# Kernel tuning notes

Hardware: AMD Instinct MI355X
Metric: run time of the kernel (lower is better)

Reference implementation:

```python
import jax, jax.numpy as jnp
import numpy as np

E = 16          # number of experts
K = 2           # top-k routing
D = 1024        # model dim
F = 512         # expert ffn dim
T = 4096        # tokens
C = 2048


def setup_inputs() -> dict:
    key = jax.random.key(0)
    k1, k2, k3, k4, k5, k6 = jax.random.split(key, 6)
    return {
        "hidden_states": jax.random.normal(k1, (T, D), jnp.float32),
        "topk_indices": jax.random.randint(k2, (T, K), 0, E, jnp.int64),
        "topk_weights": jax.random.uniform(k3, (T, K), jnp.float32),
        "w_gate": jax.random.normal(k4, (E, D, F), jnp.float32) * 0.02,
        "w_up": jax.random.normal(k5, (E, D, F), jnp.float32) * 0.02,
        "w_down": jax.random.normal(k6, (E, F, D), jnp.float32) * 0.02,
    }


def reference(hidden_states, topk_indices, topk_weights, w_gate, w_up, w_down):
    Tn, d = hidden_states.shape
    k = topk_indices.shape[1]
    TK = Tn * k

    # ---- dispatch_tokens: group (token, expert) pairs by expert id ----
    flat_e = topk_indices.reshape(-1)                 # [TK] expert id per slot
    flat_w = topk_weights.reshape(-1)                 # [TK]
    flat_t = jnp.arange(TK) // k                      # [TK] source token id
    order = jnp.argsort(flat_e)                       # sort slots by expert
    se, st, sw = flat_e[order], flat_t[order], flat_w[order]
    counts = jnp.bincount(flat_e, length=E)           # tokens per expert
    starts = jnp.cumsum(counts) - counts              # exclusive prefix sum
    pos = jnp.arange(TK) - starts[se]                 # position within expert bucket
    valid = pos < C
    slot = jnp.where(valid, se * C + pos, E * C)      # overflow -> scratch row

    # gather tokens into padded per-expert buffers [E, C, D]
    buf = jnp.zeros((E * C + 1, d), hidden_states.dtype).at[slot].set(hidden_states[st])
    xe = buf[: E * C].reshape(E, C, d)

    # ---- per-expert gated-SiLU MLP via grouped GEMMs ----
    h = jax.nn.silu(jnp.einsum('ecd,edf->ecf', xe, w_gate)) * jnp.einsum('ecd,edf->ecf', xe, w_up)
    ye = jnp.einsum('ecf,efd->ecd', h, w_down).reshape(E * C, d)

    # ---- weighted scatter-add combine (index_add_) ----
    contrib = ye[jnp.minimum(slot, E * C - 1)] * (sw * valid.astype(sw.dtype))[:, None]
    out = jnp.zeros((Tn, d), topk_weights.dtype).at[st].add(contrib)
    return out.astype(hidden_states.dtype)
```

## Files before the change

### kernel.cpp

```cpp
#include <hip/hip_runtime.h>
#include <hip/hip_bf16.h>

constexpr int E_ = 16, K_ = 2, D_ = 1024, F_ = 512, T_ = 4096;
constexpr int TK_ = T_ * K_;
constexpr int CAP_ = 2048;
constexpr int BM_ = 128;
constexpr int ROWS_MAX = 10240;

constexpr size_t SZ_W   = (size_t)E_ * F_ * D_ * 2;
constexpr size_t OFF_WGT  = 0;
constexpr size_t OFF_WUT  = OFF_WGT + SZ_W;
constexpr size_t OFF_WDT  = OFF_WUT + SZ_W;
constexpr size_t OFF_XG   = OFF_WDT + SZ_W;
constexpr size_t SZ_XG  = (size_t)ROWS_MAX * D_ * 2;
constexpr size_t OFF_H    = OFF_XG + SZ_XG;
constexpr size_t SZ_H   = (size_t)ROWS_MAX * F_ * 2;
constexpr size_t OFF_META = OFF_H + SZ_H;

typedef __attribute__((ext_vector_type(8))) short short8;
typedef __attribute__((ext_vector_type(4))) float float4v;

__device__ __forceinline__ unsigned short f2bf(float f) {
  union { float f; unsigned int u; } v; v.f = f;
  unsigned int r = (v.u + 0x7fffu + ((v.u >> 16) & 1u)) >> 16;
  return (unsigned short)r;
}

__device__ __forceinline__ void load_lds16(const unsigned short* g, unsigned short* l) {
  __builtin_amdgcn_global_load_lds(
      (const __attribute__((address_space(1))) unsigned int*)g,
      (__attribute__((address_space(3))) unsigned int*)l,
      16, 0, 0);
}

__global__ void hist_k(const int* __restrict__ idx, int* __restrict__ hist) {
  int i = blockIdx.x * blockDim.x + threadIdx.x;
  if (i < TK_) atomicAdd(&hist[idx[i]], 1);
}

__global__ void scan_k(const int* __restrict__ hist, int* __restrict__ cnt_c,
                       int* __restrict__ off_al, int* __restrict__ ctr) {
  if (threadIdx.x == 0) {
    int run = 0;
    for (int e = 0; e < E_; ++e) {
      int c = hist[e] > CAP_ ? CAP_ : hist[e];
      cnt_c[e] = c; off_al[e] = run; ctr[e] = 0;
      run += (c + BM_ - 1) & ~(BM_ - 1);
    }
  }
}

__global__ void assign_k(const int* __restrict__ idx, const float* __restrict__ tw,
                         const int* __restrict__ off_al, int* __restrict__ ctr,
                         int* __restrict__ row_token, float* __restrict__ row_weight) {
  int i = blockIdx.x * blockDim.x + threadIdx.x;
  if (i >= TK_) return;
  int e = idx[i];
  int r = atomicAdd(&ctr[e], 1);
  if (r < CAP_) {
    int row = off_al[e] + r;
    row_token[row] = i >> 1;
    row_weight[row] = tw[i];
  }
}

__global__ void gather_k(const float* __restrict__ hidden, const int* __restrict__ row_token,
                         unsigned short* __restrict__ Xg) {
  int r = blockIdx.x;
  int tok = row_token[r];
  int c = threadIdx.x * 4;
  ushort4 o;
  if (tok >= 0) {
    float4 v = *(const float4*)(hidden + (size_t)tok * D_ + c);
    o.x = f2bf(v.x); o.y = f2bf(v.y); o.z = f2bf(v.z); o.w = f2bf(v.w);
  } else {
    o.x = 0; o.y = 0; o.z = 0; o.w = 0;
  }
  *(ushort4*)(Xg + (size_t)r * D_ + c) = o;
}

__global__ void transpose_all_k(const float* __restrict__ wg, const float* __restrict__ wu,
                                const float* __restrict__ wd,
                                unsigned short* __restrict__ WgT, unsigned short* __restrict__ WuT,
                                unsigned short* __restrict__ WdT) {
  __shared__ float tile[32][33];
  int z = blockIdx.y;
  int kind = z >> 4, e = z & 15;
  int R = (kind == 2) ? F_ : D_;
  int C = (kind == 2) ? D_ : F_;
  const float* s = ((kind == 0) ? wg : (kind == 1) ? wu : wd) + (size_t)e * R * C;
  unsigned short* d = ((kind == 0) ? WgT : (kind == 1) ? WuT : WdT) + (size_t)e * R * C;
  int tilesX = C >> 5;
  int t = blockIdx.x;
  int r0 = (t / tilesX) * 32, c0 = (t % tilesX) * 32;
  int tr = threadIdx.x >> 3;
  int tc = (threadIdx.x & 7) * 4;
  float4 v = *(const float4*)(s + (size_t)(r0 + tr) * C + (c0 + tc));
  tile[tr][tc + 0] = v.x; tile[tr][tc + 1] = v.y;
  tile[tr][tc + 2] = v.z; tile[tr][tc + 3] = v.w;
  __syncthreads();
  ushort4 o;
  o.x = f2bf(tile[tc + 0][tr]);
  o.y = f2bf(tile[tc + 1][tr]);
  o.z = f2bf(tile[tc + 2][tr]);
  o.w = f2bf(tile[tc + 3][tr]);
  *(ushort4*)(d + (size_t)(c0 + tr) * R + (r0 + tc)) = o;
}


__launch_bounds__(256)
__global__ void gemm1_k(const unsigned short* __restrict__ Xg,
                        const unsigned short* __restrict__ WgT,
                        const unsigned short* __restrict__ WuT,
                        unsigned short* __restrict__ Hbuf,
                        const int* __restrict__ cnt_c, const int* __restrict__ off_al) {
  int bid = blockIdx.x;
  int swz = (bid & 7) * 512 + (bid >> 3);
  int e = swz >> 8, mt = (swz >> 3) & 31, nt = swz & 7;
  int cnt = cnt_c[e];
  if (mt * 64 >= cnt) return;
  int rbase = off_al[e] + mt * 64;

  __shared__ unsigned short lA[2][64 * 64];
  __shared__ unsigned short lBg[2][64 * 64];
  __shared__ unsigned short lBu[2][64 * 64];

  int tid = threadIdx.x, wid = tid >> 6, lane = tid & 63;
  int wm = wid >> 1, wn = wid & 1;
  int quad = lane >> 4, l15 = lane & 15;
  int sw = l15 & 7;

  const unsigned short* gA = Xg + (size_t)rbase * D_;
  const unsigned short* gB0 = WgT + ((size_t)e * F_ + nt * 64) * D_;
  const unsigned short* gB1 = WuT + ((size_t)e * F_ + nt * 64) * D_;

  float4v accg[2][2], accu[2][2];
#pragma unroll
  for (int i = 0; i < 2; ++i)
#pragma unroll
    for (int j = 0; j < 2; ++j) {
      accg[i][j] = (float4v){0.f, 0.f, 0.f, 0.f};
      accu[i][j] = (float4v){0.f, 0.f, 0.f, 0.f};
    }

  auto stage = [&](int buf, int k0) {
#pragma unroll
    for (int it = 0; it < 2; ++it) {
      int fw = it * 256 + wid * 64;
      int f = fw + lane;
      int row = f >> 3, c8 = (f & 7) ^ (row & 7);
      size_t go = (size_t)row * D_ + k0 + c8 * 8;
      load_lds16(gA + go, &lA[buf][fw * 8]);
      load_lds16(gB0 + go, &lBg[buf][fw * 8]);
      load_lds16(gB1 + go, &lBu[buf][fw * 8]);
    }
  };

  stage(0, 0);
  __syncthreads();

  for (int kt = 0; kt < 16; ++kt) {
    int cur = kt & 1;
    if (kt + 1 < 16) stage(cur ^ 1, (kt + 1) * 64);
#pragma unroll
    for (int kc = 0; kc < 2; ++kc) {
      short8 af[2], bg[2], bu[2];
#pragma unroll
      for (int i = 0; i < 2; ++i) {
        int r = wm * 32 + i * 16 + l15;
        af[i] = *(const short8*)&lA[cur][r * 64 + ((kc * 4 + quad) ^ sw) * 8];
      }
#pragma unroll
      for (int j = 0; j < 2; ++j) {
        int n = wn * 32 + j * 16 + l15;
        bg[j] = *(const short8*)&lBg[cur][n * 64 + ((kc * 4 + quad) ^ sw) * 8];
        bu[j] = *(const short8*)&lBu[cur][n * 64 + ((kc * 4 + quad) ^ sw) * 8];
      }
#pragma unroll
      for (int i = 0; i < 2; ++i)
#pragma unroll
        for (int j = 0; j < 2; ++j) {
          accg[i][j] = __builtin_amdgcn_mfma_f32_16x16x32_bf16(af[i], bg[j], accg[i][j], 0, 0, 0);
          accu[i][j] = __builtin_amdgcn_mfma_f32_16x16x32_bf16(af[i], bu[j], accu[i][j], 0, 0, 0);
        }
    }
    __syncthreads();
  }

  int rem = cnt - mt * 64;
#pragma unroll
  for (int i = 0; i < 2; ++i)
#pragma unroll
    for (int j = 0; j < 2; ++j)
#pragma unroll
      for (int r = 0; r < 4; ++r) {
        int row = wm * 32 + i * 16 + quad * 4 + r;
        if (row < rem) {
          float g = accg[i][j][r], u = accu[i][j][r];
          float h = (g / (1.f + __expf(-g))) * u;
          int n = nt * 64 + wn * 32 + j * 16 + l15;
          Hbuf[(size_t)(rbase + row) * F_ + n] = f2bf(h);
        }
      }
}

__launch_bounds__(256)
__global__ void gemm2_k(const unsigned short* __restrict__ Hbuf,
                        const unsigned short* __restrict__ WdT,
                        float* __restrict__ out,
                        const int* __restrict__ cnt_c, const int* __restrict__ off_al,
                        const int* __restrict__ row_token, const float* __restrict__ row_weight) {
  int bid = blockIdx.x;
  int swz = (bid & 7) * 512 + (bid >> 3);
  int e = swz >> 8, mt = (swz >> 3) & 31, nt = swz & 7;
  int cnt = cnt_c[e];
  if (mt * 64 >= cnt) return;
  int rbase = off_al[e] + mt * 64;

  __shared__ unsigned short lA[2][64 * 64];
  __shared__ unsigned short lB[2][128 * 64];

  int tid = threadIdx.x, wid = tid >> 6, lane = tid & 63;
  int wm = wid >> 1, wn = wid & 1;
  int quad = lane >> 4, l15 = lane & 15;
  int sw = l15 & 7;

  const unsigned short* gA = Hbuf + (size_t)rbase * F_;
  const unsigned short* gB = WdT + ((size_t)e * D_ + nt * 128) * F_;

  float4v acc[2][4];
#pragma unroll
  for (int i = 0; i < 2; ++i)
#pragma unroll
    for (int j = 0; j < 4; ++j) acc[i][j] = (float4v){0.f, 0.f, 0.f, 0.f};

  auto stage = [&](int buf, int k0) {
#pragma unroll
    for (int it = 0; it < 2; ++it) {
      int fw = it * 256 + wid * 64;
      int f = fw + lane;
      int row = f >> 3, c8 = (f & 7) ^ (row & 7);
      load_lds16(gA + (size_t)row * F_ + k0 + c8 * 8, &lA[buf][fw * 8]);
    }
#pragma unroll
    for (int it = 0; it < 4; ++it) {
      int fw = it * 256 + wid * 64;
      int f = fw + lane;
      int row = f >> 3, c8 = (f & 7) ^ (row & 7);
      load_lds16(gB + (size_t)row * F_ + k0 + c8 * 8, &lB[buf][fw * 8]);
    }
  };

  stage(0, 0);
  __syncthreads();

  for (int kt = 0; kt < 8; ++kt) {
    int cur = kt & 1;
    if (kt + 1 < 8) stage(cur ^ 1, (kt + 1) * 64);
#pragma unroll
    for (int kc = 0; kc < 2; ++kc) {
      short8 af[2], bf[4];
#pragma unroll
      for (int i = 0; i < 2; ++i) {
        int r = wm * 32 + i * 16 + l15;
        af[i] = *(const short8*)&lA[cur][r * 64 + ((kc * 4 + quad) ^ sw) * 8];
      }
#pragma unroll
      for (int j = 0; j < 4; ++j) {
        int n = wn * 64 + j * 16 + l15;
        bf[j] = *(const short8*)&lB[cur][n * 64 + ((kc * 4 + quad) ^ sw) * 8];
      }
#pragma unroll
      for (int i = 0; i < 2; ++i)
#pragma unroll
        for (int j = 0; j < 4; ++j)
          acc[i][j] = __builtin_amdgcn_mfma_f32_16x16x32_bf16(af[i], bf[j], acc[i][j], 0, 0, 0);
    }
    __syncthreads();
  }

  int rem = cnt - mt * 64;
#pragma unroll
  for (int i = 0; i < 2; ++i)
#pragma unroll
    for (int r = 0; r < 4; ++r) {
      int row = wm * 32 + i * 16 + quad * 4 + r;
      if (row < rem) {
        int gr = rbase + row;
        int tok = row_token[gr];
        if (tok >= 0) {
          float w = row_weight[gr];
          float* op = out + (size_t)tok * D_;
#pragma unroll
          for (int j = 0; j < 4; ++j) {
            int n = nt * 128 + wn * 64 + j * 16 + l15;
            atomicAdd(op + n, w * acc[i][j][r]);
          }
        }
      }
    }
}

extern "C" void kernel_launch(void* const* d_in, const int* in_sizes, int n_in,
                              void* d_out, int out_size, void* d_ws, size_t ws_size,
                              hipStream_t stream) {
  const float* hidden  = (const float*)d_in[0];
  const int*   topkidx = (const int*)d_in[1];
  const float* topkw   = (const float*)d_in[2];
  const float* w_gate  = (const float*)d_in[3];
  const float* w_up    = (const float*)d_in[4];
  const float* w_down  = (const float*)d_in[5];
  float* out = (float*)d_out;

  char* ws = (char*)d_ws;
  unsigned short* WgT = (unsigned short*)(ws + OFF_WGT);
  unsigned short* WuT = (unsigned short*)(ws + OFF_WUT);
  unsigned short* WdT = (unsigned short*)(ws + OFF_WDT);
  unsigned short* Xg  = (unsigned short*)(ws + OFF_XG);
  unsigned short* Hb  = (unsigned short*)(ws + OFF_H);
  int* meta           = (int*)(ws + OFF_META);
  int* cnt_c     = meta;
  int* off_al    = meta + 16;
  int* row_token = meta + 32;
  float* row_weight = (float*)(meta + 32 + ROWS_MAX);
  int* hist      = meta + 32 + 2 * ROWS_MAX;
  int* ctr       = hist + 16;

  hipMemsetAsync(out, 0, (size_t)out_size * sizeof(float), stream);
  hipMemsetAsync(hist, 0, 16 * sizeof(int), stream);
  hipMemsetAsync(row_token, 0xFF, (size_t)ROWS_MAX * sizeof(int), stream);

  hist_k<<<TK_ / 256, 256, 0, stream>>>(topkidx, hist);
  scan_k<<<1, 64, 0, stream>>>(hist, cnt_c, off_al, ctr);
  assign_k<<<TK_ / 256, 256, 0, stream>>>(topkidx, topkw, off_al, ctr, row_token, row_weight);

  transpose_all_k<<<dim3(512, 48), 256, 0, stream>>>(w_gate, w_up, w_down, WgT, WuT, WdT);
  gather_k<<<ROWS_MAX, 256, 0, stream>>>(hidden, row_token, Xg);

  gemm1_k<<<4096, 256, 0, stream>>>(Xg, WgT, WuT, Hb, cnt_c, off_al);
  gemm2_k<<<4096, 256, 0, stream>>>(Hb, WdT, out, cnt_c, off_al, row_token, row_weight);
}
```

Baseline: 290.4 us.

## Fuse dispatch kernels, widen weight transpose tiles, replace atomic combine with gather

Merges the histogram, scan and assign kernels and the memsets into one single-block dispatch kernel that also records each slot's row. The weight transpose moves to 64x64 tiles with 16-byte bf16 stores. gemm2 now writes plain fp32 expert outputs into a buffer that reuses the gate/up weight region, and a new per-token combine kernel applies the routing weights. This drops the output memset and the fp32 atomics, at the cost of an extra full fp32 write and read of the expert outputs plus one more launch. The single-block dispatch serialises the routing work.

```diff
diff --git a/kernel.cpp b/kernel.cpp
--- a/kernel.cpp
+++ b/kernel.cpp
@@ -8,14 +8,16 @@
 constexpr int ROWS_MAX = 10240;
 
 constexpr size_t SZ_W   = (size_t)E_ * F_ * D_ * 2;
-constexpr size_t OFF_WGT  = 0;
+constexpr size_t OFF_WDT  = 0;
+constexpr size_t OFF_WGT  = OFF_WDT + SZ_W;
 constexpr size_t OFF_WUT  = OFF_WGT + SZ_W;
-constexpr size_t OFF_WDT  = OFF_WUT + SZ_W;
-constexpr size_t OFF_XG   = OFF_WDT + SZ_W;
+constexpr size_t OFF_XG   = OFF_WUT + SZ_W;
 constexpr size_t SZ_XG  = (size_t)ROWS_MAX * D_ * 2;
 constexpr size_t OFF_H    = OFF_XG + SZ_XG;
 constexpr size_t SZ_H   = (size_t)ROWS_MAX * F_ * 2;
 constexpr size_t OFF_META = OFF_H + SZ_H;
+constexpr size_t OFF_YE   = OFF_WGT;
+static_assert(OFF_YE + (size_t)ROWS_MAX * D_ * 4 <= OFF_H, "Ye overlaps live buffers");
 
 typedef __attribute__((ext_vector_type(8))) short short8;
 typedef __attribute__((ext_vector_type(4))) float float4v;
@@ -33,34 +35,38 @@
       16, 0, 0);
 }
 
-__global__ void hist_k(const int* __restrict__ idx, int* __restrict__ hist) {
-  int i = blockIdx.x * blockDim.x + threadIdx.x;
-  if (i < TK_) atomicAdd(&hist[idx[i]], 1);
-}
-
-__global__ void scan_k(const int* __restrict__ hist, int* __restrict__ cnt_c,
-                       int* __restrict__ off_al, int* __restrict__ ctr) {
-  if (threadIdx.x == 0) {
+__launch_bounds__(1024)
+__global__ void dispatch_k(const int* __restrict__ idx, const float* __restrict__ tw,
+                           int* __restrict__ cnt_c, int* __restrict__ off_al,
+                           int* __restrict__ row_token, float* __restrict__ row_weight,
+                           int* __restrict__ slot_row) {
+  __shared__ int hist[E_], offs[E_], ctr[E_];
+  int tid = threadIdx.x;
+  if (tid < E_) hist[tid] = 0;
+  __syncthreads();
+  for (int i = tid; i < TK_; i += 1024) atomicAdd(&hist[idx[i]], 1);
+  __syncthreads();
+  if (tid == 0) {
     int run = 0;
     for (int e = 0; e < E_; ++e) {
       int c = hist[e] > CAP_ ? CAP_ : hist[e];
-      cnt_c[e] = c; off_al[e] = run; ctr[e] = 0;
+      cnt_c[e] = c; off_al[e] = run; offs[e] = run; ctr[e] = 0;
       run += (c + BM_ - 1) & ~(BM_ - 1);
     }
   }
-}
-
-__global__ void assign_k(const int* __restrict__ idx, const float* __restrict__ tw,
-                         const int* __restrict__ off_al, int* __restrict__ ctr,
-                         int* __restrict__ row_token, float* __restrict__ row_weight) {
-  int i = blockIdx.x * blockDim.x + threadIdx.x;
-  if (i >= TK_) return;
-  int e = idx[i];
-  int r = atomicAdd(&ctr[e], 1);
-  if (r < CAP_) {
-    int row = off_al[e] + r;
-    row_token[row] = i >> 1;
-    row_weight[row] = tw[i];
+  __syncthreads();
+  for (int r = tid; r < ROWS_MAX; r += 1024) row_token[r] = -1;
+  __syncthreads();
+  for (int i = tid; i < TK_; i += 1024) {
+    int e = idx[i];
+    int r = atomicAdd(&ctr[e], 1);
+    int row = -1;
+    if (r < CAP_) {
+      row = offs[e] + r;
+      row_token[row] = i >> 1;
+      row_weight[row] = tw[i];
+    }
+    slot_row[i] = row;
   }
 }
 
@@ -79,32 +85,43 @@
   *(ushort4*)(Xg + (size_t)r * D_ + c) = o;
 }
 
+__launch_bounds__(256)
 __global__ void transpose_all_k(const float* __restrict__ wg, const float* __restrict__ wu,
                                 const float* __restrict__ wd,
                                 unsigned short* __restrict__ WgT, unsigned short* __restrict__ WuT,
                                 unsigned short* __restrict__ WdT) {
-  __shared__ float tile[32][33];
+  __shared__ float tile[64][65];
   int z = blockIdx.y;
   int kind = z >> 4, e = z & 15;
   int R = (kind == 2) ? F_ : D_;
   int C = (kind == 2) ? D_ : F_;
   const float* s = ((kind == 0) ? wg : (kind == 1) ? wu : wd) + (size_t)e * R * C;
   unsigned short* d = ((kind == 0) ? WgT : (kind == 1) ? WuT : WdT) + (size_t)e * R * C;
-  int tilesX = C >> 5;
+  int tilesX = C >> 6;
   int t = blockIdx.x;
-  int r0 = (t / tilesX) * 32, c0 = (t % tilesX) * 32;
-  int tr = threadIdx.x >> 3;
-  int tc = (threadIdx.x & 7) * 4;
-  float4 v = *(const float4*)(s + (size_t)(r0 + tr) * C + (c0 + tc));
-  tile[tr][tc + 0] = v.x; tile[tr][tc + 1] = v.y;
-  tile[tr][tc + 2] = v.z; tile[tr][tc + 3] = v.w;
-  __syncthreads();
-  ushort4 o;
-  o.x = f2bf(tile[tc + 0][tr]);
-  o.y = f2bf(tile[tc + 1][tr]);
-  o.z = f2bf(tile[tc + 2][tr]);
-  o.w = f2bf(tile[tc + 3][tr]);
-  *(ushort4*)(d + (size_t)(c0 + tr) * R + (r0 + tc)) = o;
+  int r0 = (t / tilesX) * 64, c0 = (t % tilesX) * 64;
+
+  int lr = threadIdx.x >> 4;
+  int lc = (threadIdx.x & 15) * 4;
+#pragma unroll
+  for (int it = 0; it < 4; ++it) {
+    int row = lr + it * 16;
+    float4 v = *(const float4*)(s + (size_t)(r0 + row) * C + (c0 + lc));
+    tile[row][lc + 0] = v.x; tile[row][lc + 1] = v.y;
+    tile[row][lc + 2] = v.z; tile[row][lc + 3] = v.w;
+  }
+  __syncthreads();
+
+  int w = threadIdx.x >> 6, l = threadIdx.x & 63;
+#pragma unroll
+  for (int it = 0; it < 2; ++it) {
+    int c = (it * 4 + w) * 8 + (l >> 3);
+    int r8 = (l & 7) * 8;
+    short8 o;
+#pragma unroll
+    for (int j = 0; j < 8; ++j) o[j] = (short)f2bf(tile[r8 + j][c]);
+    *(short8*)(d + (size_t)(c0 + c) * R + (r0 + r8)) = o;
+  }
 }
 
 
@@ -207,9 +224,8 @@
 __launch_bounds__(256)
 __global__ void gemm2_k(const unsigned short* __restrict__ Hbuf,
                         const unsigned short* __restrict__ WdT,
-                        float* __restrict__ out,
-                        const int* __restrict__ cnt_c, const int* __restrict__ off_al,
-                        const int* __restrict__ row_token, const float* __restrict__ row_weight) {
+                        float* __restrict__ Ye,
+                        const int* __restrict__ cnt_c, const int* __restrict__ off_al) {
   int bid = blockIdx.x;
   int swz = (bid & 7) * 512 + (bid >> 3);
   int e = swz >> 8, mt = (swz >> 3) & 31, nt = swz & 7;
@@ -286,19 +302,30 @@
     for (int r = 0; r < 4; ++r) {
       int row = wm * 32 + i * 16 + quad * 4 + r;
       if (row < rem) {
-        int gr = rbase + row;
-        int tok = row_token[gr];
-        if (tok >= 0) {
-          float w = row_weight[gr];
-          float* op = out + (size_t)tok * D_;
-#pragma unroll
-          for (int j = 0; j < 4; ++j) {
-            int n = nt * 128 + wn * 64 + j * 16 + l15;
-            atomicAdd(op + n, w * acc[i][j][r]);
-          }
-        }
-      }
-    }
+        float* yp = Ye + (size_t)(rbase + row) * D_ + nt * 128 + wn * 64 + l15;
+#pragma unroll
+        for (int j = 0; j < 4; ++j) yp[j * 16] = acc[i][j][r];
+      }
+    }
+}
+
+__global__ void combine_k(const float* __restrict__ Ye, const int* __restrict__ slot_row,
+                          const float* __restrict__ row_weight, float* __restrict__ out) {
+  int t = blockIdx.x;
+  int c = threadIdx.x * 4;
+  int r0 = slot_row[2 * t], r1 = slot_row[2 * t + 1];
+  float4 acc = {0.f, 0.f, 0.f, 0.f};
+  if (r0 >= 0) {
+    float w = row_weight[r0];
+    float4 y = *(const float4*)(Ye + (size_t)r0 * D_ + c);
+    acc.x = w * y.x; acc.y = w * y.y; acc.z = w * y.z; acc.w = w * y.w;
+  }
+  if (r1 >= 0) {
+    float w = row_weight[r1];
+    float4 y = *(const float4*)(Ye + (size_t)r1 * D_ + c);
+    acc.x += w * y.x; acc.y += w * y.y; acc.z += w * y.z; acc.w += w * y.w;
+  }
+  *(float4*)(out + (size_t)t * D_ + c) = acc;
 }
 
 extern "C" void kernel_launch(void* const* d_in, const int* in_sizes, int n_in,
@@ -313,30 +340,25 @@
   float* out = (float*)d_out;
 
   char* ws = (char*)d_ws;
+  unsigned short* WdT = (unsigned short*)(ws + OFF_WDT);
   unsigned short* WgT = (unsigned short*)(ws + OFF_WGT);
   unsigned short* WuT = (unsigned short*)(ws + OFF_WUT);
-  unsigned short* WdT = (unsigned short*)(ws + OFF_WDT);
   unsigned short* Xg  = (unsigned short*)(ws + OFF_XG);
   unsigned short* Hb  = (unsigned short*)(ws + OFF_H);
+  float* Ye           = (float*)(ws + OFF_YE);
   int* meta           = (int*)(ws + OFF_META);
   int* cnt_c     = meta;
   int* off_al    = meta + 16;
   int* row_token = meta + 32;
   float* row_weight = (float*)(meta + 32 + ROWS_MAX);
-  int* hist      = meta + 32 + 2 * ROWS_MAX;
-  int* ctr       = hist + 16;
-
-  hipMemsetAsync(out, 0, (size_t)out_size * sizeof(float), stream);
-  hipMemsetAsync(hist, 0, 16 * sizeof(int), stream);
-  hipMemsetAsync(row_token, 0xFF, (size_t)ROWS_MAX * sizeof(int), stream);
-
-  hist_k<<<TK_ / 256, 256, 0, stream>>>(topkidx, hist);
-  scan_k<<<1, 64, 0, stream>>>(hist, cnt_c, off_al, ctr);
-  assign_k<<<TK_ / 256, 256, 0, stream>>>(topkidx, topkw, off_al, ctr, row_token, row_weight);
-
-  transpose_all_k<<<dim3(512, 48), 256, 0, stream>>>(w_gate, w_up, w_down, WgT, WuT, WdT);
+  int* slot_row  = meta + 32 + 2 * ROWS_MAX;
+
+  dispatch_k<<<1, 1024, 0, stream>>>(topkidx, topkw, cnt_c, off_al, row_token, row_weight,
+                                     slot_row);
+  transpose_all_k<<<dim3(128, 48), 256, 0, stream>>>(w_gate, w_up, w_down, WgT, WuT, WdT);
   gather_k<<<ROWS_MAX, 256, 0, stream>>>(hidden, row_token, Xg);
 
   gemm1_k<<<4096, 256, 0, stream>>>(Xg, WgT, WuT, Hb, cnt_c, off_al);
-  gemm2_k<<<4096, 256, 0, stream>>>(Hb, WdT, out, cnt_c, off_al, row_token, row_weight);
-}
+  gemm2_k<<<4096, 256, 0, stream>>>(Hb, WdT, Ye, cnt_c, off_al);
+  combine_k<<<T_, 256, 0, stream>>>(Ye, slot_row, row_weight, out);
+}
```

Result: faster. 237.5 us (-18.2%).
